# Optimization experiments

Hardware: AMD Instinct MI355X
Metric: run time of the kernel (lower is better)

Reference implementation:

```python
import jax, jax.numpy as jnp
import numpy as np

N = 50000
E = 1600000
IN_CH = 34
HID = 64
OUT = 64
NEG_SLOPE = 0.2


def _gat_layer(x, src, dst, W, a_src, a_dst, bias, heads, out_ch, concat):
    n = x.shape[0]
    xw = (x @ W).reshape(n, heads, out_ch)                      # [N,H,C]
    al_src = jnp.sum(xw * a_src[None], axis=-1)                  # [N,H]
    al_dst = jnp.sum(xw * a_dst[None], axis=-1)                  # [N,H]
    e = jax.nn.leaky_relu(al_src[src] + al_dst[dst], NEG_SLOPE)  # [E,H]
    # segment softmax over incoming edges of each dst node (self-loops ensure non-empty)
    m = jax.ops.segment_max(e, dst, num_segments=n)              # [N,H]
    ex = jnp.exp(e - m[dst])
    denom = jax.ops.segment_sum(ex, dst, num_segments=n)         # [N,H]
    alpha = ex / denom[dst]                                      # [E,H]
    msg = xw[src] * alpha[:, :, None]                            # [E,H,C]
    out = jax.ops.segment_sum(msg, dst, num_segments=n)          # [N,H,C]
    if concat:
        out = out.reshape(n, heads * out_ch)
    else:
        out = out.mean(axis=1)
    return out + bias


def setup_inputs() -> dict:
    key = jax.random.key(0)
    ks = jax.random.split(key, 12)
    x = jax.random.normal(ks[0], (N, IN_CH), dtype=jnp.float32)
    edge_index = jax.random.randint(ks[1], (2, E), 0, N, dtype=jnp.int64)
    # layer 1: heads=2, concat -> 128
    W1 = jax.random.normal(ks[2], (IN_CH, 2 * HID), dtype=jnp.float32) * 0.1
    a_src1 = jax.random.normal(ks[3], (2, HID), dtype=jnp.float32) * 0.1
    a_dst1 = jax.random.normal(ks[4], (2, HID), dtype=jnp.float32) * 0.1
    b1 = jnp.zeros((2 * HID,), dtype=jnp.float32)
    # layer 2: heads=1, mean
    W2 = jax.random.normal(ks[5], (2 * HID, OUT), dtype=jnp.float32) * 0.1
    a_src2 = jax.random.normal(ks[6], (1, OUT), dtype=jnp.float32) * 0.1
    a_dst2 = jax.random.normal(ks[7], (1, OUT), dtype=jnp.float32) * 0.1
    b2 = jnp.zeros((OUT,), dtype=jnp.float32)
    return {"x": x, "edge_index": edge_index, "W1": W1, "a_src1": a_src1,
            "a_dst1": a_dst1, "b1": b1, "W2": W2, "a_src2": a_src2,
            "a_dst2": a_dst2, "b2": b2}


def reference(x, edge_index, W1, a_src1, a_dst1, b1, W2, a_src2, a_dst2, b2):
    n = x.shape[0]
    loops = jnp.arange(n, dtype=edge_index.dtype)
    src = jnp.concatenate([edge_index[0], loops])  # PyG GATConv add_self_loops=True
    dst = jnp.concatenate([edge_index[1], loops])
    h = _gat_layer(x, src, dst, W1, a_src1, a_dst1, b1, heads=2, out_ch=HID, concat=True)
    h = jax.nn.relu(h)
    out = _gat_layer(h, src, dst, W2, a_src2, a_dst2, b2, heads=1, out_ch=OUT, concat=False)
    return out
```

## Files before the change

kernel.cpp:

```cpp
#include <hip/hip_runtime.h>
#include <math.h>

#define N_NODES 50000
#define E_EDGES 1600000
#define IN_CH   34
#define NEG     0.2f
#define NB      196
#define CAP     10000

typedef __attribute__((ext_vector_type(2))) float fv2;

static __device__ __forceinline__ unsigned short f2bf(float f) {
    unsigned int u = __float_as_uint(f);
    u += 0x7fffu + ((u >> 16) & 1u);
    return (unsigned short)(u >> 16);
}
static __device__ __forceinline__ float bflo(unsigned int u) {
    return __uint_as_float(u << 16);
}
static __device__ __forceinline__ float bfhi(unsigned int u) {
    return __uint_as_float(u & 0xffff0000u);
}
static __device__ __forceinline__ float lrelu_exp(float e) {
    return expf(e > 0.f ? e : NEG * e);
}

static __device__ __forceinline__ int scan256_excl(int v, int* wsum) {
    const int lane = threadIdx.x & 63, wv = threadIdx.x >> 6;
    int x = v;
    #pragma unroll
    for (int off = 1; off < 64; off <<= 1) {
        int y = __shfl_up(x, off);
        if (lane >= off) x += y;
    }
    if (lane == 63) wsum[wv] = x;
    __syncthreads();
    if (threadIdx.x < 4) {
        int s = wsum[threadIdx.x];
        #pragma unroll
        for (int off = 1; off < 4; off <<= 1) {
            int y = __shfl_up(s, off);
            if ((int)threadIdx.x >= off) s += y;
        }
        wsum[threadIdx.x] = s;
    }
    __syncthreads();
    const int woff = wv ? wsum[wv - 1] : 0;
    return woff + x - v;
}

__global__ __launch_bounds__(256) void k_bin(
    const int* __restrict__ srcA, const int* __restrict__ dstA,
    int* __restrict__ gcur, unsigned int* __restrict__ binned)
{
    __shared__ unsigned int raw[4096];
    __shared__ unsigned short rnk[4096];
    __shared__ int cnt[256], cur[256];
    const int tid = threadIdx.x;
    cnt[tid] = 0;
    __syncthreads();
    const int base = blockIdx.x * 4096;
    #pragma unroll
    for (int i = 0; i < 16; ++i) {
        const int e = base + i * 256 + tid;
        if (e < E_EDGES) {
            const int d = dstA[e], s = srcA[e];
            raw[i * 256 + tid] = ((unsigned int)d << 16) | (unsigned int)s;
            rnk[i * 256 + tid] = (unsigned short)atomicAdd(&cnt[d >> 8], 1);
        }
    }
    __syncthreads();
    const int v = cnt[tid];
    cur[tid] = (tid < NB && v > 0) ? (tid * CAP + atomicAdd(&gcur[tid], v)) : 0;
    __syncthreads();
    const int mE = min(4096, E_EDGES - base);
    for (int p = tid; p < mE; p += 256) {
        const unsigned int u = raw[p];
        binned[cur[u >> 24] + rnk[p]] = u;
    }
}

__global__ __launch_bounds__(256) void k_fine(
    const int* __restrict__ gcur, const unsigned int* __restrict__ binned,
    int2* __restrict__ rowspan, unsigned short* __restrict__ sorted_src)
{
    __shared__ unsigned int sbin[CAP];
    __shared__ unsigned short rnk[CAP];
    __shared__ int cnt[256], sbase[256];
    __shared__ int wsum[4];
    const int tid = threadIdx.x;
    const int b = blockIdx.x;
    const int bbase = b * CAP;
    const int cntb = gcur[b];
    cnt[tid] = 0;
    __syncthreads();
    for (int p = tid; p < cntb; p += 256) {
        const unsigned int u = binned[bbase + p];
        sbin[p] = u;
        rnk[p] = (unsigned short)atomicAdd(&cnt[(u >> 16) & 255], 1);
    }
    __syncthreads();
    const int v = cnt[tid];
    const int excl = scan256_excl(v, wsum);
    const int node = b * 256 + tid;
    if (node < N_NODES) rowspan[node] = make_int2(bbase + excl, bbase + excl + v);
    sbase[tid] = excl;
    __syncthreads();
    for (int p = tid; p < cntb; p += 256) {
        const unsigned int u = sbin[p];
        sorted_src[bbase + sbase[(u >> 16) & 255] + rnk[p]] =
            (unsigned short)(u & 0xffffu);
    }
}

__global__ __launch_bounds__(256) void k_node1(
    const float* __restrict__ x, const float* __restrict__ W1,
    const float* __restrict__ a_src, const float* __restrict__ a_dst,
    unsigned short* __restrict__ xw1b,
    float* __restrict__ al_s, float* __restrict__ al_d,
    const float* __restrict__ W2, unsigned int* __restrict__ w2p)
{
    __shared__ float sW[IN_CH * 132];
    __shared__ float sx[32 * 35];
    __shared__ float sas[128], sad[128];
    const int tid = threadIdx.x;
    if (blockIdx.x == 0) {
        for (int i = tid; i < 4096; i += 256) {
            const int k2 = i >> 6, c = i & 63;
            const unsigned int lo = f2bf(W2[(2 * k2) * 64 + c]);
            const unsigned int hi = f2bf(W2[(2 * k2 + 1) * 64 + c]);
            w2p[i] = lo | (hi << 16);
        }
    }
    for (int i = tid; i < IN_CH * 128; i += 256) {
        int k = i >> 7, c = i & 127;
        sW[k * 132 + c] = W1[i];
    }
    if (tid < 128) { sas[tid] = a_src[tid]; sad[tid] = a_dst[tid]; }
    const int n0 = blockIdx.x * 32;
    for (int i = tid; i < 32 * IN_CH; i += 256) {
        int n = i / IN_CH;
        sx[n * 35 + (i - n * IN_CH)] = (n0 + n < N_NODES) ? x[n0 * IN_CH + i] : 0.f;
    }
    __syncthreads();

    const int tc = tid & 31, tn = tid >> 5;
    float acc[4][4] = {{0.f}};
    for (int k = 0; k < IN_CH; ++k) {
        const float4 wv = *reinterpret_cast<const float4*>(&sW[k * 132 + 4 * tc]);
        #pragma unroll
        for (int j = 0; j < 4; ++j) {
            const float hj = sx[(4 * tn + j) * 35 + k];
            acc[j][0] += hj * wv.x; acc[j][1] += hj * wv.y;
            acc[j][2] += hj * wv.z; acc[j][3] += hj * wv.w;
        }
    }
    #pragma unroll
    for (int j = 0; j < 4; ++j) {
        const int node = n0 + 4 * tn + j;
        float ps = 0.f, pd = 0.f;
        #pragma unroll
        for (int c = 0; c < 4; ++c) {
            ps += acc[j][c] * sas[4 * tc + c];
            pd += acc[j][c] * sad[4 * tc + c];
        }
        #pragma unroll
        for (int off = 1; off < 16; off <<= 1) {
            ps += __shfl_xor(ps, off);
            pd += __shfl_xor(pd, off);
        }
        if (node < N_NODES) {
            if ((tc & 15) == 0) {
                int h = tc >> 4;
                al_s[node * 2 + h] = ps;
                al_d[node * 2 + h] = pd;
            }
            ushort4 u;
            u.x = f2bf(acc[j][0]); u.y = f2bf(acc[j][1]);
            u.z = f2bf(acc[j][2]); u.w = f2bf(acc[j][3]);
            *reinterpret_cast<ushort4*>(&xw1b[node * 128 + 4 * tc]) = u;
        }
    }
}

__global__ __launch_bounds__(256) void k_gather1(
    const int2* __restrict__ rowspan, const unsigned short* __restrict__ sorted_src,
    const unsigned int* __restrict__ xw1u,
    const float* __restrict__ al_s, const float* __restrict__ al_d,
    const float* __restrict__ b1, const unsigned int* __restrict__ w2p,
    const float* __restrict__ as2, const float* __restrict__ ad2,
    unsigned short* __restrict__ xw2b,
    float* __restrict__ al_s2, float* __restrict__ al_d2)
{
    __shared__ unsigned int sW2[4096];
    __shared__ float4 AB[2][4][32];
    __shared__ float2 sh2[4][64];
    const int tid = threadIdx.x;
    for (int i = tid; i < 4096; i += 256) sW2[i] = w2p[i];
    __syncthreads();

    const int wave = tid >> 6;
    const int lane = tid & 63;
    const int node = blockIdx.x * 4 + wave;
    const int2 span = rowspan[node];
    const int head = lane >> 5;

    const float2 ald  = *reinterpret_cast<const float2*>(&al_d[node * 2]);
    const float2 als0 = *reinterpret_cast<const float2*>(&al_s[node * 2]);
    const float w0h0 = lrelu_exp(als0.x + ald.x);
    const float w0h1 = lrelu_exp(als0.y + ald.y);
    const float wself = head ? w0h1 : w0h0;

    const unsigned int su = xw1u[node * 64 + lane];
    fv2 accX = { wself * bflo(su), wself * bfhi(su) };
    fv2 accY = { 0.f, 0.f };
    float dv0 = 0.f, dv1 = 0.f;
    const float4* ABh = AB[head][wave];

    for (int base = span.x; base < span.y; base += 64) {
        const int rem = span.y - base;
        const int m = rem < 64 ? rem : 64;
        const int mp = (m + 1) & ~1;
        if (lane < m) {
            const int s = sorted_src[base + lane];
            const float2 als = *reinterpret_cast<const float2*>(&al_s[s * 2]);
            const float w0 = lrelu_exp(als.x + ald.x);
            const float w1 = lrelu_exp(als.y + ald.y);
            dv0 += w0; dv1 += w1;
            const float offf = __int_as_float(s << 6);
            ((float2*)&AB[0][wave][lane >> 1])[lane & 1] = make_float2(offf, w0);
            ((float2*)&AB[1][wave][lane >> 1])[lane & 1] = make_float2(offf, w1);
        } else if (lane < mp) {
            const float offf = __int_as_float(node << 6);
            ((float2*)&AB[0][wave][lane >> 1])[lane & 1] = make_float2(offf, 0.f);
            ((float2*)&AB[1][wave][lane >> 1])[lane & 1] = make_float2(offf, 0.f);
        }
        const int P = mp >> 1;
        int p = 0;
        for (; p + 4 <= P; p += 4) {
            const float4 q0 = ABh[p + 0];
            const float4 q1 = ABh[p + 1];
            const float4 q2 = ABh[p + 2];
            const float4 q3 = ABh[p + 3];
            const unsigned int a0 = xw1u[__float_as_int(q0.x) + lane];
            const unsigned int b0 = xw1u[__float_as_int(q0.z) + lane];
            const unsigned int a1 = xw1u[__float_as_int(q1.x) + lane];
            const unsigned int b1v = xw1u[__float_as_int(q1.z) + lane];
            const unsigned int a2 = xw1u[__float_as_int(q2.x) + lane];
            const unsigned int b2 = xw1u[__float_as_int(q2.z) + lane];
            const unsigned int a3 = xw1u[__float_as_int(q3.x) + lane];
            const unsigned int b3 = xw1u[__float_as_int(q3.z) + lane];
            fv2 f;
            f.x = bflo(a0); f.y = bfhi(a0); accX += f * q0.y;
            f.x = bflo(b0); f.y = bfhi(b0); accY += f * q0.w;
            f.x = bflo(a1); f.y = bfhi(a1); accX += f * q1.y;
            f.x = bflo(b1v); f.y = bfhi(b1v); accY += f * q1.w;
            f.x = bflo(a2); f.y = bfhi(a2); accX += f * q2.y;
            f.x = bflo(b2); f.y = bfhi(b2); accY += f * q2.w;
            f.x = bflo(a3); f.y = bfhi(a3); accX += f * q3.y;
            f.x = bflo(b3); f.y = bfhi(b3); accY += f * q3.w;
        }
        for (; p < P; ++p) {
            const float4 q = ABh[p];
            const unsigned int a = xw1u[__float_as_int(q.x) + lane];
            const unsigned int b = xw1u[__float_as_int(q.z) + lane];
            fv2 f;
            f.x = bflo(a); f.y = bfhi(a); accX += f * q.y;
            f.x = bflo(b); f.y = bfhi(b); accY += f * q.w;
        }
    }
    accX += accY;
    #pragma unroll
    for (int off = 32; off; off >>= 1) {
        dv0 += __shfl_xor(dv0, off);
        dv1 += __shfl_xor(dv1, off);
    }
    const float den = head ? (dv1 + w0h1) : (dv0 + w0h0);
    const float2 bv = *reinterpret_cast<const float2*>(&b1[2 * lane]);
    float o0 = accX.x / den + bv.x;
    float o1 = accX.y / den + bv.y;
    o0 = o0 > 0.f ? o0 : 0.f;
    o1 = o1 > 0.f ? o1 : 0.f;

    sh2[wave][lane] = make_float2(o0, o1);
    float a2acc = 0.f;
    #pragma unroll 4
    for (int k2 = 0; k2 < 64; ++k2) {
        const float2 hp = sh2[wave][k2];
        const unsigned int wv2 = sW2[k2 * 64 + lane];
        a2acc += hp.x * bflo(wv2) + hp.y * bfhi(wv2);
    }
    float ps2 = a2acc * as2[lane];
    float pd2 = a2acc * ad2[lane];
    #pragma unroll
    for (int off = 32; off; off >>= 1) {
        ps2 += __shfl_xor(ps2, off);
        pd2 += __shfl_xor(pd2, off);
    }
    xw2b[node * 64 + lane] = f2bf(a2acc);
    if (lane == 0) { al_s2[node] = ps2; al_d2[node] = pd2; }
}

__global__ __launch_bounds__(256) void k_gather2(
    const int2* __restrict__ rowspan, const unsigned short* __restrict__ sorted_src,
    const unsigned int* __restrict__ xw2u,
    const float* __restrict__ al_s, const float* __restrict__ al_d,
    const float* __restrict__ b2, float* __restrict__ out)
{
    __shared__ float4 AB[4][32];
    const int wave = threadIdx.x >> 6;
    const int lane = threadIdx.x & 63;
    const int node = blockIdx.x * 4 + wave;
    const int2 span = rowspan[node];
    const int li = lane & 31, hsel = lane >> 5;

    const float ald = al_d[node];
    const float w0s = lrelu_exp(al_s[node] + ald);
    const unsigned int su = xw2u[node * 32 + li];
    const float wself = hsel ? 0.f : w0s;
    fv2 acc = { wself * bflo(su), wself * bfhi(su) };
    float dv = 0.f;
    const float4* ABw = AB[wave];

    for (int base = span.x; base < span.y; base += 64) {
        const int rem = span.y - base;
        const int m = rem < 64 ? rem : 64;
        const int mp = (m + 3) & ~3;
        if (lane < m) {
            const int s = sorted_src[base + lane];
            const float w = lrelu_exp(al_s[s] + ald);
            dv += w;
            ((float2*)&AB[wave][lane >> 1])[lane & 1] =
                make_float2(__int_as_float(s << 5), w);
        } else if (lane < mp) {
            ((float2*)&AB[wave][lane >> 1])[lane & 1] =
                make_float2(__int_as_float(node << 5), 0.f);
        }
        const int P = mp >> 1;
        int p = hsel;
        for (; p + 2 < P; p += 4) {
            const float4 qA = ABw[p];
            const float4 qB = ABw[p + 2];
            const unsigned int aA = xw2u[__float_as_int(qA.x) + li];
            const unsigned int bA = xw2u[__float_as_int(qA.z) + li];
            const unsigned int aB = xw2u[__float_as_int(qB.x) + li];
            const unsigned int bB = xw2u[__float_as_int(qB.z) + li];
            fv2 f;
            f.x = bflo(aA); f.y = bfhi(aA); acc += f * qA.y;
            f.x = bflo(bA); f.y = bfhi(bA); acc += f * qA.w;
            f.x = bflo(aB); f.y = bfhi(aB); acc += f * qB.y;
            f.x = bflo(bB); f.y = bfhi(bB); acc += f * qB.w;
        }
        for (; p < P; p += 2) {
            const float4 q = ABw[p];
            const unsigned int a = xw2u[__float_as_int(q.x) + li];
            const unsigned int b = xw2u[__float_as_int(q.z) + li];
            fv2 f;
            f.x = bflo(a); f.y = bfhi(a); acc += f * q.y;
            f.x = bflo(b); f.y = bfhi(b); acc += f * q.w;
        }
    }
    acc.x += __shfl_xor(acc.x, 32);
    acc.y += __shfl_xor(acc.y, 32);
    #pragma unroll
    for (int off = 32; off; off >>= 1) dv += __shfl_xor(dv, off);
    if (lane < 32) {
        const float den = dv + w0s;
        const float2 bv = *reinterpret_cast<const float2*>(&b2[2 * li]);
        *reinterpret_cast<float2*>(&out[node * 64 + 2 * li]) =
            make_float2(acc.x / den + bv.x, acc.y / den + bv.y);
    }
}

extern "C" void kernel_launch(void* const* d_in, const int* in_sizes, int n_in,
                              void* d_out, int out_size, void* d_ws, size_t ws_size,
                              hipStream_t stream)
{
    const float* x   = (const float*)d_in[0];
    const int*   ei  = (const int*)d_in[1];
    const float* W1  = (const float*)d_in[2];
    const float* as1 = (const float*)d_in[3];
    const float* ad1 = (const float*)d_in[4];
    const float* b1  = (const float*)d_in[5];
    const float* W2  = (const float*)d_in[6];
    const float* as2 = (const float*)d_in[7];
    const float* ad2 = (const float*)d_in[8];
    const float* b2  = (const float*)d_in[9];
    float* out = (float*)d_out;

    const int* srcA = ei;
    const int* dstA = ei + E_EDGES;

    char* ws = (char*)d_ws;
    int2*           rowspan    = (int2*)(ws);
    unsigned short* sorted_src = (unsigned short*)(ws + 409600);
    int*            gcur       = (int*)(ws + 4341760);
    float*          al_s1      = (float*)(ws + 4343808);
    float*          al_d1      = (float*)(ws + 4753408);
    float*          al_s2      = (float*)(ws + 5163008);
    float*          al_d2      = (float*)(ws + 5367808);
    unsigned short* xw1b       = (unsigned short*)(ws + 5572608);
    unsigned int*   binned     = (unsigned int*)(ws + 18376704);
    unsigned short* xw2b       = (unsigned short*)(ws + 26220544);
    unsigned int*   w2p        = (unsigned int*)(ws + 32620544);

    hipMemsetAsync(gcur, 0, NB * sizeof(int), stream);
    hipLaunchKernelGGL(k_bin, dim3((E_EDGES + 4095) / 4096), dim3(256), 0, stream,
                       srcA, dstA, gcur, binned);
    hipLaunchKernelGGL(k_node1, dim3((N_NODES + 31) / 32), dim3(256), 0, stream,
                       x, W1, as1, ad1, xw1b, al_s1, al_d1, W2, w2p);
    hipLaunchKernelGGL(k_fine, dim3(NB), dim3(256), 0, stream,
                       gcur, binned, rowspan, sorted_src);
    hipLaunchKernelGGL(k_gather1, dim3(N_NODES / 4), dim3(256), 0, stream,
                       rowspan, sorted_src, (const unsigned int*)xw1b,
                       al_s1, al_d1, b1, w2p, as2, ad2, xw2b, al_s2, al_d2);
    hipLaunchKernelGGL(k_gather2, dim3(N_NODES / 4), dim3(256), 0, stream,
                       rowspan, sorted_src, (const unsigned int*)xw2b,
                       al_s2, al_d2, b2, out);
}
```

Before: 272.9 us.

## Split layer-2 projection out of gather1 into tiled k_node2 and deepen gather unrolling

Moves the second-layer linear transform and attention-logit computation out of the layer-1 gather kernel into a separate register-tiled GEMM kernel that reads a float32 hidden buffer. gather1 no longer stages 16KB of W2 in shared memory or runs a per-node 64x64 dot loop, which lowers its LDS use and should allow higher occupancy. The gather loops in both gather kernels are unrolled further so more independent loads are in flight per wave. The cost is an extra kernel launch plus a 25.6MB float32 write and read of the hidden activations, and W2 is now used in full precision instead of bf16.

```diff
diff --git a/kernel.cpp b/kernel.cpp
--- a/kernel.cpp
+++ b/kernel.cpp
@@ -117,21 +117,12 @@
     const float* __restrict__ x, const float* __restrict__ W1,
     const float* __restrict__ a_src, const float* __restrict__ a_dst,
     unsigned short* __restrict__ xw1b,
-    float* __restrict__ al_s, float* __restrict__ al_d,
-    const float* __restrict__ W2, unsigned int* __restrict__ w2p)
+    float* __restrict__ al_s, float* __restrict__ al_d)
 {
     __shared__ float sW[IN_CH * 132];
     __shared__ float sx[32 * 35];
     __shared__ float sas[128], sad[128];
     const int tid = threadIdx.x;
-    if (blockIdx.x == 0) {
-        for (int i = tid; i < 4096; i += 256) {
-            const int k2 = i >> 6, c = i & 63;
-            const unsigned int lo = f2bf(W2[(2 * k2) * 64 + c]);
-            const unsigned int hi = f2bf(W2[(2 * k2 + 1) * 64 + c]);
-            w2p[i] = lo | (hi << 16);
-        }
-    }
     for (int i = tid; i < IN_CH * 128; i += 256) {
         int k = i >> 7, c = i & 127;
         sW[k * 132 + c] = W1[i];
@@ -187,20 +178,11 @@
     const int2* __restrict__ rowspan, const unsigned short* __restrict__ sorted_src,
     const unsigned int* __restrict__ xw1u,
     const float* __restrict__ al_s, const float* __restrict__ al_d,
-    const float* __restrict__ b1, const unsigned int* __restrict__ w2p,
-    const float* __restrict__ as2, const float* __restrict__ ad2,
-    unsigned short* __restrict__ xw2b,
-    float* __restrict__ al_s2, float* __restrict__ al_d2)
-{
-    __shared__ unsigned int sW2[4096];
+    const float* __restrict__ b1, float* __restrict__ hbuf)
+{
     __shared__ float4 AB[2][4][32];
-    __shared__ float2 sh2[4][64];
-    const int tid = threadIdx.x;
-    for (int i = tid; i < 4096; i += 256) sW2[i] = w2p[i];
-    __syncthreads();
-
-    const int wave = tid >> 6;
-    const int lane = tid & 63;
+    const int wave = threadIdx.x >> 6;
+    const int lane = threadIdx.x & 63;
     const int node = blockIdx.x * 4 + wave;
     const int2 span = rowspan[node];
     const int head = lane >> 5;
@@ -237,28 +219,22 @@
         }
         const int P = mp >> 1;
         int p = 0;
-        for (; p + 4 <= P; p += 4) {
-            const float4 q0 = ABh[p + 0];
-            const float4 q1 = ABh[p + 1];
-            const float4 q2 = ABh[p + 2];
-            const float4 q3 = ABh[p + 3];
-            const unsigned int a0 = xw1u[__float_as_int(q0.x) + lane];
-            const unsigned int b0 = xw1u[__float_as_int(q0.z) + lane];
-            const unsigned int a1 = xw1u[__float_as_int(q1.x) + lane];
-            const unsigned int b1v = xw1u[__float_as_int(q1.z) + lane];
-            const unsigned int a2 = xw1u[__float_as_int(q2.x) + lane];
-            const unsigned int b2 = xw1u[__float_as_int(q2.z) + lane];
-            const unsigned int a3 = xw1u[__float_as_int(q3.x) + lane];
-            const unsigned int b3 = xw1u[__float_as_int(q3.z) + lane];
-            fv2 f;
-            f.x = bflo(a0); f.y = bfhi(a0); accX += f * q0.y;
-            f.x = bflo(b0); f.y = bfhi(b0); accY += f * q0.w;
-            f.x = bflo(a1); f.y = bfhi(a1); accX += f * q1.y;
-            f.x = bflo(b1v); f.y = bfhi(b1v); accY += f * q1.w;
-            f.x = bflo(a2); f.y = bfhi(a2); accX += f * q2.y;
-            f.x = bflo(b2); f.y = bfhi(b2); accY += f * q2.w;
-            f.x = bflo(a3); f.y = bfhi(a3); accX += f * q3.y;
-            f.x = bflo(b3); f.y = bfhi(b3); accY += f * q3.w;
+        for (; p + 8 <= P; p += 8) {
+            float4 q[8];
+            #pragma unroll
+            for (int t = 0; t < 8; ++t) q[t] = ABh[p + t];
+            unsigned int va[8], vb[8];
+            #pragma unroll
+            for (int t = 0; t < 8; ++t) {
+                va[t] = xw1u[__float_as_int(q[t].x) + lane];
+                vb[t] = xw1u[__float_as_int(q[t].z) + lane];
+            }
+            #pragma unroll
+            for (int t = 0; t < 8; ++t) {
+                fv2 f;
+                f.x = bflo(va[t]); f.y = bfhi(va[t]); accX += f * q[t].y;
+                f.x = bflo(vb[t]); f.y = bfhi(vb[t]); accY += f * q[t].w;
+            }
         }
         for (; p < P; ++p) {
             const float4 q = ABh[p];
@@ -281,24 +257,60 @@
     float o1 = accX.y / den + bv.y;
     o0 = o0 > 0.f ? o0 : 0.f;
     o1 = o1 > 0.f ? o1 : 0.f;
-
-    sh2[wave][lane] = make_float2(o0, o1);
-    float a2acc = 0.f;
-    #pragma unroll 4
-    for (int k2 = 0; k2 < 64; ++k2) {
-        const float2 hp = sh2[wave][k2];
-        const unsigned int wv2 = sW2[k2 * 64 + lane];
-        a2acc += hp.x * bflo(wv2) + hp.y * bfhi(wv2);
-    }
-    float ps2 = a2acc * as2[lane];
-    float pd2 = a2acc * ad2[lane];
-    #pragma unroll
-    for (int off = 32; off; off >>= 1) {
-        ps2 += __shfl_xor(ps2, off);
-        pd2 += __shfl_xor(pd2, off);
-    }
-    xw2b[node * 64 + lane] = f2bf(a2acc);
-    if (lane == 0) { al_s2[node] = ps2; al_d2[node] = pd2; }
+    *reinterpret_cast<float2*>(&hbuf[node * 128 + 2 * lane]) = make_float2(o0, o1);
+}
+
+__global__ __launch_bounds__(256) void k_node2(
+    const float* __restrict__ hbuf, const float* __restrict__ W2,
+    const float* __restrict__ a_src, const float* __restrict__ a_dst,
+    unsigned short* __restrict__ xw2b, float* __restrict__ al_s, float* __restrict__ al_d)
+{
+    __shared__ float sW[128 * 64];
+    __shared__ float sh[64 * 129];
+    __shared__ float sas[64], sad[64];
+    const int tid = threadIdx.x;
+    for (int i = tid; i < 128 * 64; i += 256) sW[i] = W2[i];
+    if (tid < 64) { sas[tid] = a_src[tid]; sad[tid] = a_dst[tid]; }
+    const int n0 = blockIdx.x * 64;
+    for (int i = tid; i < 64 * 128; i += 256) {
+        int n = i >> 7, c = i & 127;
+        sh[n * 129 + c] = (n0 + n < N_NODES) ? hbuf[(long)(n0 + n) * 128 + c] : 0.f;
+    }
+    __syncthreads();
+
+    const int tc = tid & 15, tn = tid >> 4;
+    float acc[4][4] = {{0.f}};
+    for (int k = 0; k < 128; ++k) {
+        const float4 wv = *reinterpret_cast<const float4*>(&sW[k * 64 + 4 * tc]);
+        #pragma unroll
+        for (int j = 0; j < 4; ++j) {
+            const float hj = sh[(4 * tn + j) * 129 + k];
+            acc[j][0] += hj * wv.x; acc[j][1] += hj * wv.y;
+            acc[j][2] += hj * wv.z; acc[j][3] += hj * wv.w;
+        }
+    }
+    #pragma unroll
+    for (int j = 0; j < 4; ++j) {
+        const int node = n0 + 4 * tn + j;
+        float ps = 0.f, pd = 0.f;
+        #pragma unroll
+        for (int c = 0; c < 4; ++c) {
+            ps += acc[j][c] * sas[4 * tc + c];
+            pd += acc[j][c] * sad[4 * tc + c];
+        }
+        #pragma unroll
+        for (int off = 1; off < 16; off <<= 1) {
+            ps += __shfl_xor(ps, off);
+            pd += __shfl_xor(pd, off);
+        }
+        if (node < N_NODES) {
+            if (tc == 0) { al_s[node] = ps; al_d[node] = pd; }
+            ushort4 u;
+            u.x = f2bf(acc[j][0]); u.y = f2bf(acc[j][1]);
+            u.z = f2bf(acc[j][2]); u.w = f2bf(acc[j][3]);
+            *reinterpret_cast<ushort4*>(&xw2b[node * 64 + 4 * tc]) = u;
+        }
+    }
 }
 
 __global__ __launch_bounds__(256) void k_gather2(
@@ -338,18 +350,22 @@
         }
         const int P = mp >> 1;
         int p = hsel;
-        for (; p + 2 < P; p += 4) {
-            const float4 qA = ABw[p];
-            const float4 qB = ABw[p + 2];
-            const unsigned int aA = xw2u[__float_as_int(qA.x) + li];
-            const unsigned int bA = xw2u[__float_as_int(qA.z) + li];
-            const unsigned int aB = xw2u[__float_as_int(qB.x) + li];
-            const unsigned int bB = xw2u[__float_as_int(qB.z) + li];
-            fv2 f;
-            f.x = bflo(aA); f.y = bfhi(aA); acc += f * qA.y;
-            f.x = bflo(bA); f.y = bfhi(bA); acc += f * qA.w;
-            f.x = bflo(aB); f.y = bfhi(aB); acc += f * qB.y;
-            f.x = bflo(bB); f.y = bfhi(bB); acc += f * qB.w;
+        for (; p + 6 < P; p += 8) {
+            float4 q[4];
+            q[0] = ABw[p];     q[1] = ABw[p + 2];
+            q[2] = ABw[p + 4]; q[3] = ABw[p + 6];
+            unsigned int va[4], vb[4];
+            #pragma unroll
+            for (int t = 0; t < 4; ++t) {
+                va[t] = xw2u[__float_as_int(q[t].x) + li];
+                vb[t] = xw2u[__float_as_int(q[t].z) + li];
+            }
+            #pragma unroll
+            for (int t = 0; t < 4; ++t) {
+                fv2 f;
+                f.x = bflo(va[t]); f.y = bfhi(va[t]); acc += f * q[t].y;
+                f.x = bflo(vb[t]); f.y = bfhi(vb[t]); acc += f * q[t].w;
+            }
         }
         for (; p < P; p += 2) {
             const float4 q = ABw[p];
@@ -402,18 +418,20 @@
     unsigned short* xw1b       = (unsigned short*)(ws + 5572608);
     unsigned int*   binned     = (unsigned int*)(ws + 18376704);
     unsigned short* xw2b       = (unsigned short*)(ws + 26220544);
-    unsigned int*   w2p        = (unsigned int*)(ws + 32620544);
+    float*          hbuf       = (float*)(ws + 32624640);
 
     hipMemsetAsync(gcur, 0, NB * sizeof(int), stream);
     hipLaunchKernelGGL(k_bin, dim3((E_EDGES + 4095) / 4096), dim3(256), 0, stream,
                        srcA, dstA, gcur, binned);
     hipLaunchKernelGGL(k_node1, dim3((N_NODES + 31) / 32), dim3(256), 0, stream,
-                       x, W1, as1, ad1, xw1b, al_s1, al_d1, W2, w2p);
+                       x, W1, as1, ad1, xw1b, al_s1, al_d1);
     hipLaunchKernelGGL(k_fine, dim3(NB), dim3(256), 0, stream,
                        gcur, binned, rowspan, sorted_src);
     hipLaunchKernelGGL(k_gather1, dim3(N_NODES / 4), dim3(256), 0, stream,
                        rowspan, sorted_src, (const unsigned int*)xw1b,
-                       al_s1, al_d1, b1, w2p, as2, ad2, xw2b, al_s2, al_d2);
+                       al_s1, al_d1, b1, hbuf);
+    hipLaunchKernelGGL(k_node2, dim3((N_NODES + 63) / 64), dim3(256), 0, stream,
+                       hbuf, W2, as2, ad2, xw2b, al_s2, al_d2);
     hipLaunchKernelGGL(k_gather2, dim3(N_NODES / 4), dim3(256), 0, stream,
                        rowspan, sorted_src, (const unsigned int*)xw2b,
                        al_s2, al_d2, b2, out);
```

Measured after the change: 281.9 us. 1.03x slower.
